# Kernel optimization log

Hardware: AMD Instinct MI355X
Metric: run time of the kernel (lower is better)

## Reference

```python
import jax, jax.numpy as jnp
import numpy as np
from jax import lax

P_BOX, N_PTS, K_MAX, HID, SAMP = 512, 50000, 64, 256, 4
C_IMG, HF, WF = 96, 160, 512
IMG_W, IMG_H = 1280.0, 384.0
OFFSET_SCALE = 0.04
PT_IN = 7


def _lin(key, fan_in, fan_out):
    return jax.random.normal(key, (fan_in, fan_out), dtype=jnp.float32) / np.sqrt(fan_in)


def setup_inputs() -> dict:
    key = jax.random.key(0)
    ks = jax.random.split(key, 24)
    xy = jax.random.uniform(ks[0], (N_PTS, 2), minval=-40.0, maxval=40.0)
    z = jax.random.uniform(ks[1], (N_PTS, 1), minval=-2.0, maxval=4.0)
    feats = jax.random.normal(ks[2], (N_PTS, 4))
    points = jnp.concatenate([xy, z, feats], axis=-1).astype(jnp.float32)
    ctr_xy = jax.random.uniform(ks[3], (P_BOX, 2), minval=-35.0, maxval=35.0)
    ctr_z = jax.random.uniform(ks[4], (P_BOX, 1), minval=-1.0, maxval=2.0)
    dxy = jax.random.uniform(ks[5], (P_BOX, 2), minval=2.0, maxval=6.0)
    dz = jax.random.uniform(ks[6], (P_BOX, 1), minval=1.0, maxval=3.0)
    yaw = jax.random.uniform(ks[7], (P_BOX, 1), minval=-np.pi, maxval=np.pi)
    boxes = jnp.concatenate([ctr_xy, ctr_z, dxy, dz, yaw], axis=-1).astype(jnp.float32)
    image_feat = jax.random.normal(ks[8], (1, C_IMG, HF, WF), dtype=jnp.float32)
    fx = fy = 400.0
    proj = jnp.array([[IMG_W / 2, -fx, 0.0, 0.0], [IMG_H / 2, 0.0, -fy, 0.0], [1.0, 0.0, 0.0, 0.0]], dtype=jnp.float32)
    return {
        'points': points, 'boxes': boxes, 'image_feat': image_feat, 'proj': proj,
        'pe_w1': _lin(ks[9], PT_IN + 1, HID), 'pe_b1': jnp.zeros((HID,), jnp.float32),
        'pe_w2': _lin(ks[10], HID, HID), 'pe_b2': jnp.zeros((HID,), jnp.float32),
        'q_w': _lin(ks[11], HID, HID), 'q_b': jnp.zeros((HID,), jnp.float32),
        'f_w': _lin(ks[12], C_IMG, HID), 'f_b': jnp.zeros((HID,), jnp.float32),
        'off_w': _lin(ks[13], HID, SAMP * 2), 'off_b': jnp.zeros((SAMP * 2,), jnp.float32),
        'wt_w': _lin(ks[14], HID, SAMP), 'wt_b': jnp.zeros((SAMP,), jnp.float32),
        'o_w1': _lin(ks[15], 2 * HID, HID), 'o_b1': jnp.zeros((HID,), jnp.float32),
        'o_w2': _lin(ks[16], HID, HID), 'o_b2': jnp.zeros((HID,), jnp.float32),
        'score_w': _lin(ks[17], HID, 1), 'score_b': jnp.zeros((1,), jnp.float32),
    }


def _fused_features(points, boxes, image_feat, proj, pe_w1, pe_b1, pe_w2, pe_b2,
                    q_w, q_b, f_w, f_b, off_w, off_b, wt_w, wt_b,
                    o_w1, o_b1, o_w2, o_b2, score_w, score_b):
    NEG = jnp.float32(-1e30)
    xyz = points[:, :3]
    ctr, dims, yaw = boxes[:, :3], boxes[:, 3:6], boxes[:, 6]
    c, s = jnp.cos(yaw)[:, None], jnp.sin(yaw)[:, None]
    rel = xyz[None, :, :] - ctr[:, None, :]                      # [P,N,3]
    lx = rel[..., 0] * c + rel[..., 1] * s                       # box-frame coords
    ly = -rel[..., 0] * s + rel[..., 1] * c
    lz = rel[..., 2]
    half = dims[:, None, :] * 0.5
    inside = (jnp.abs(lx) <= half[..., 0]) & (jnp.abs(ly) <= half[..., 1]) & (jnp.abs(lz) <= half[..., 2])
    counts = inside.sum(axis=1)                                  # [P]
    d = jnp.maximum(dims, 1e-3)[:, None, :]
    nx, ny, nz = lx / d[..., 0], ly / d[..., 1], lz / d[..., 2] - 0.5
    planar = jnp.where(inside, jnp.sqrt(nx * nx + ny * ny), jnp.inf)
    _, idx = lax.top_k(-planar, K_MAX)                           # K closest inside points
    slot_valid = jnp.arange(K_MAX)[None, :] < counts[:, None]    # [P,K]
    take = lambda a: jnp.take_along_axis(a, idx, axis=1)
    nl = jnp.stack([take(nx), take(ny), take(nz)], axis=-1)      # [P,K,3]
    nl = jnp.where(slot_valid[..., None], nl, 0.0)
    pts_sel = jnp.where(slot_valid[..., None], points[idx], 0.0)  # [P,K,7]
    # local density: knn(4) mean distance, excluding self
    diff = nl[:, :, None, :] - nl[:, None, :, :]
    dmat = jnp.sqrt((diff * diff).sum(-1) + 1e-12)               # [P,K,K]
    dmat = jnp.where(slot_valid[:, None, :], dmat, jnp.inf)
    knn = -lax.top_k(-dmat, 4)[0]                                # 4 smallest, col0 = self
    m = jnp.minimum(counts, K_MAX)
    col_ok = jnp.arange(1, 4)[None, None, :] < jnp.minimum(m, 4)[:, None, None]
    nb = jnp.where(col_ok, knn[:, :, 1:], 0.0)
    n_nb = jnp.maximum(jnp.minimum(m, 4) - 1, 1).astype(nl.dtype)
    density = jnp.where(slot_valid, jnp.exp(-nb.sum(-1) / n_nb[:, None]), 0.0)  # [P,K]
    tokens = jnp.concatenate([nl, pts_sel[:, :, 3:PT_IN], density[..., None]], axis=-1)  # [P,K,8]
    h = jnp.maximum(tokens @ pe_w1 + pe_b1, 0.0) @ pe_w2 + pe_b2  # point encoder [P,K,H]
    # project points to normalized image coords
    hom = pts_sel[:, :, :3] @ proj[:, :3].T + proj[:, 3]
    depth = hom[..., 2]
    safe_d = jnp.where(jnp.abs(depth) > 1e-3, depth, 1e-3)
    rx = 2.0 * (hom[..., 0] / safe_d) / (IMG_W - 1.0) - 1.0
    ry = 2.0 * (hom[..., 1] / safe_d) / (IMG_H - 1.0) - 1.0
    ref = jnp.stack([rx, ry], axis=-1)                           # [P,K,2]
    valid = (depth > 0.1) & (jnp.abs(rx) <= 1.0) & (jnp.abs(ry) <= 1.0) & slot_valid
    # cross-modal deformable attention (lite)
    q = h @ q_w + q_b
    fm = jnp.einsum('chw,cd->dhw', image_feat[0], f_w) + f_b[:, None, None]  # [H,Hf,Wf]
    offs = (jnp.tanh(h @ off_w + off_b)).reshape(P_BOX, K_MAX, SAMP, 2) * OFFSET_SCALE
    w = jax.nn.softmax(h @ wt_w + wt_b, axis=-1)                 # [P,K,S]
    grid = jnp.clip(ref[:, :, None, :] + offs, -1.2, 1.2)
    px = (grid[..., 0] + 1.0) * 0.5 * (WF - 1)                   # align_corners=True
    py = (grid[..., 1] + 1.0) * 0.5 * (HF - 1)
    x0, y0 = jnp.floor(px), jnp.floor(py)

    def gather(xi, yi):
        inb = (xi >= 0) & (xi <= WF - 1) & (yi >= 0) & (yi <= HF - 1)
        xc = jnp.clip(xi, 0, WF - 1).astype(jnp.int32)
        yc = jnp.clip(yi, 0, HF - 1).astype(jnp.int32)
        return fm[:, yc, xc] * inb[None].astype(fm.dtype)        # [H,P,K,S]

    wx1, wy1 = px - x0, py - y0
    samp = (gather(x0, y0) * (1 - wx1) * (1 - wy1) + gather(x0 + 1, y0) * wx1 * (1 - wy1)
            + gather(x0, y0 + 1) * (1 - wx1) * wy1 + gather(x0 + 1, y0 + 1) * wx1 * wy1)
    samp = jnp.moveaxis(samp, 0, -1)                             # [P,K,S,H]
    vm = valid.astype(h.dtype)
    samp = samp * vm[:, :, None, None]
    w = w * vm[:, :, None]
    w = w / jnp.maximum(w.sum(-1, keepdims=True), 1e-6)
    context = (samp * w[..., None]).sum(axis=2) * vm[..., None]  # [P,K,H]
    cat = jnp.concatenate([q * vm[..., None], context], axis=-1)
    img_tok = jnp.maximum(cat @ o_w1 + o_b1, 0.0) @ o_w2 + o_b2
    fused = h + img_tok                                          # [P,K,H]
    # masked attention pooling over valid slots
    logits = (fused @ score_w + score_b).squeeze(-1)
    logits = jnp.where(slot_valid, logits, NEG)
    valid_rows = slot_valid.any(axis=1)
    logits = jnp.where(valid_rows[:, None], logits, 0.0)
    pw = jnp.where(valid_rows[:, None], jax.nn.softmax(logits, axis=-1), 0.0)
    pooled = jnp.einsum('pk,pkd->pd', pw, fused)                 # [P,H]
    return pooled, counts.astype(jnp.float32)[:, None]


def reference(points, boxes, image_feat, proj, pe_w1, pe_b1, pe_w2, pe_b2,
              q_w, q_b, f_w, f_b, off_w, off_b, wt_w, wt_b,
              o_w1, o_b1, o_w2, o_b2, score_w, score_b):
    return _fused_features(points, boxes, image_feat, proj, pe_w1, pe_b1, pe_w2, pe_b2,
                           q_w, q_b, f_w, f_b, off_w, off_b, wt_w, wt_b,
                           o_w1, o_b1, o_w2, o_b2, score_w, score_b)
```

## Files before the change

### kernel.cpp

```cpp
#include <hip/hip_runtime.h>
#include <hip/hip_bf16.h>

#define P_BOX 512
#define NP    50000
#define NPAD  50176
#define KM    64
#define NKEY  4096
#define HF    160
#define WF    512

typedef unsigned long long u64;
typedef unsigned short u16;
typedef unsigned int u32;
typedef __attribute__((ext_vector_type(8))) short short8;
typedef __attribute__((ext_vector_type(4))) float f32x4;

__device__ __forceinline__ u16 f2bf(float f) {
  u32 u = __float_as_uint(f);
  u32 r = u + 0x7fffu + ((u >> 16) & 1u);
  return (u16)(r >> 16);
}
__device__ __forceinline__ float bf2f(u16 h) { return __uint_as_float(((u32)h) << 16); }
__device__ __forceinline__ float bfl(u32 u) { return __uint_as_float(u << 16); }
__device__ __forceinline__ float bfh(u32 u) { return __uint_as_float(u & 0xffff0000u); }

__device__ __forceinline__ int aIdx(int m, int d) {
  return m * 256 + (((d >> 3) ^ (m & 7)) << 3) + (d & 7);
}
__device__ __forceinline__ const short8* aGr(const u16* A, int m, int g) {
  return (const short8*)(A + m * 256 + ((g ^ (m & 7)) << 3));
}

__launch_bounds__(512)
__global__ void k_prep(const float* __restrict__ pts, const float* __restrict__ img,
                       const float* __restrict__ q_w, const float* __restrict__ q_b,
                       const float* __restrict__ f_w, const float* __restrict__ f_b,
                       const float* __restrict__ o_w1, const float* __restrict__ pe_w1,
                       const float* __restrict__ pe_w2, const float* __restrict__ o_w2,
                       const float* __restrict__ off_w, const float* __restrict__ wt_w,
                       const float* __restrict__ off_b, const float* __restrict__ wt_b,
                       float* __restrict__ xs, float* __restrict__ ys, float* __restrict__ zs,
                       u16* __restrict__ pe_w2T, u16* __restrict__ WqT,
                       u16* __restrict__ o_w2T, u16* __restrict__ FoT,
                       u16* __restrict__ HWT, u16* __restrict__ pe_w1T,
                       float* __restrict__ bq, float* __restrict__ fbo,
                       float* __restrict__ hb, u16* __restrict__ imgT) {
  __shared__ __align__(16) char smem[99840];
  const int blk = blockIdx.x;
  const int t = threadIdx.x;

  if (blk < 160) {
    const int h = blk;
    u16* tile = (u16*)smem;
#pragma unroll 4
    for (int it = 0; it < 24; ++it) {
      int idx = it * 512 + t;
      int c = idx >> 7, w4 = idx & 127;
      float4 v = ((const float4*)(img + ((size_t)(c * HF + h)) * WF))[w4];
      ushort4 o;
      o.x = f2bf(v.x); o.y = f2bf(v.y); o.z = f2bf(v.z); o.w = f2bf(v.w);
      *(ushort4*)(tile + c * 520 + w4 * 4) = o;
    }
    __syncthreads();
#pragma unroll 2
    for (int it = 0; it < 12; ++it) {
      int idx = it * 512 + t;
      int w = idx / 12, cq = idx % 12;
      const u16* tp = tile + (cq * 8) * 520 + w;
      u32 p0 = (u32)tp[0] | ((u32)tp[520] << 16);
      u32 p1 = (u32)tp[1040] | ((u32)tp[1560] << 16);
      u32 p2 = (u32)tp[2080] | ((u32)tp[2600] << 16);
      u32 p3 = (u32)tp[3120] | ((u32)tp[3640] << 16);
      ((uint4*)(imgT + ((size_t)(h * WF + w)) * 96))[cq] = make_uint4(p0, p1, p2, p3);
    }
  } else if (blk < 185) {
    int g = blk - 160;
#pragma unroll
    for (int r = 0; r < 4; ++r) {
      int i = g * 2048 + r * 512 + t;
      if (i < NPAD) {
        if (i < NP) {
          xs[i] = pts[i * 7 + 0];
          ys[i] = pts[i * 7 + 1];
          zs[i] = pts[i * 7 + 2];
        } else {
          xs[i] = 1e9f; ys[i] = 1e9f; zs[i] = 1e9f;
        }
      }
    }
  } else if (blk < 209) {
    int gg = blk - 185;
    const bool isWq = gg < 16;
    const int g = isWq ? gg : gg - 16;
    const int n0 = (g & 3) * 64;
    const int x0 = (g >> 2) * 64;
    float* sA = (float*)smem;
    float* sB = (float*)smem + 64 * 65;
    float acc[2][4];
#pragma unroll
    for (int r = 0; r < 2; ++r)
#pragma unroll
      for (int c = 0; c < 4; ++c) acc[r][c] = 0.f;
    const int tx = t & 15, ty = t >> 4;
    for (int j0 = 0; j0 < 256; j0 += 64) {
      {
        int nn = t & 63, jb = t >> 6;
#pragma unroll
        for (int r = 0; r < 8; ++r) {
          int jj = jb + r * 8;
          int row = (isWq ? 0 : 256) + j0 + jj;
          sA[jj * 65 + nn] = o_w1[row * 256 + n0 + nn];
        }
      }
      {
        int jj = t & 63, xb = t >> 6;
#pragma unroll
        for (int r = 0; r < 8; ++r) {
          int xx = xb + r * 8;
          float v = 0.f;
          if (isWq) v = q_w[(x0 + xx) * 256 + j0 + jj];
          else if (x0 + xx < 96) v = f_w[(x0 + xx) * 256 + j0 + jj];
          sB[jj * 65 + xx] = v;
        }
      }
      __syncthreads();
#pragma unroll 8
      for (int jj = 0; jj < 64; ++jj) {
        float a[2], b[4];
#pragma unroll
        for (int r = 0; r < 2; ++r) a[r] = sA[jj * 65 + ty * 2 + r];
#pragma unroll
        for (int c = 0; c < 4; ++c) b[c] = sB[jj * 65 + tx * 4 + c];
#pragma unroll
        for (int r = 0; r < 2; ++r)
#pragma unroll
          for (int c = 0; c < 4; ++c) acc[r][c] += a[r] * b[c];
      }
      __syncthreads();
    }
    if (isWq) {
#pragma unroll
      for (int r = 0; r < 2; ++r) {
        ushort4 o;
        o.x = f2bf(acc[r][0]); o.y = f2bf(acc[r][1]);
        o.z = f2bf(acc[r][2]); o.w = f2bf(acc[r][3]);
        *(ushort4*)(WqT + (size_t)(n0 + ty * 2 + r) * 256 + x0 + tx * 4) = o;
      }
    } else if (x0 + tx * 4 < 96) {
#pragma unroll
      for (int r = 0; r < 2; ++r) {
        ushort4 o;
        o.x = f2bf(acc[r][0]); o.y = f2bf(acc[r][1]);
        o.z = f2bf(acc[r][2]); o.w = f2bf(acc[r][3]);
        *(ushort4*)(FoT + (size_t)(n0 + ty * 2 + r) * 96 + x0 + tx * 4) = o;
      }
    }
  } else if (blk < 241) {
    int g = blk - 209;
    const float* src = (g < 16) ? pe_w2 : o_w2;
    u16* dst = (g < 16) ? pe_w2T : o_w2T;
    int tile_ = g & 15;
    int n0 = (tile_ & 3) * 64, k0 = (tile_ >> 2) * 64;
    float* shf = (float*)smem;
    {
      int nn = t & 63, kb = t >> 6;
#pragma unroll
      for (int r = 0; r < 8; ++r) {
        int kk = kb + r * 8;
        shf[kk * 65 + nn] = src[(k0 + kk) * 256 + n0 + nn];
      }
    }
    __syncthreads();
    {
      int kk = t & 63, nb = t >> 6;
#pragma unroll
      for (int r = 0; r < 8; ++r) {
        int nn = nb + r * 8;
        dst[(size_t)(n0 + nn) * 256 + k0 + kk] = f2bf(shf[kk * 65 + nn]);
      }
    }
  } else {
    if (t < 256) {
      int n = t;
      float a1 = 0.f, a2 = 0.f;
      for (int j = 0; j < 256; ++j) {
        a1 += q_b[j] * o_w1[j * 256 + n];
        a2 += f_b[j] * o_w1[(256 + j) * 256 + n];
      }
      bq[n] = a1;
      fbo[n] = a2;
#pragma unroll
      for (int s = 0; s < 16; ++s) {
        float v = (s < 8) ? off_w[n * 8 + s] : ((s < 12) ? wt_w[n * 4 + (s - 8)] : 0.f);
        HWT[s * 256 + n] = f2bf(v);
      }
#pragma unroll
      for (int k = 0; k < 32; ++k)
        pe_w1T[n * 32 + k] = (k < 8) ? f2bf(pe_w1[k * 256 + n]) : (u16)0;
      if (t < 16) hb[t] = (t < 8) ? off_b[t] : ((t < 12) ? wt_b[t - 8] : 0.f);
    }
  }
}

__launch_bounds__(512)
__global__ void k_sel(const float* __restrict__ pts, const float* __restrict__ boxes,
                      const float* __restrict__ proj,
                      const float* __restrict__ xs, const float* __restrict__ ys,
                      const float* __restrict__ zs,
                      uint4* __restrict__ TOK, float* __restrict__ VM,
                      float* __restrict__ REF, int* __restrict__ CNT,
                      float* __restrict__ out) {
  __shared__ u64 keys[NKEY];
  __shared__ u64 keys2[KM];
  __shared__ float s_nl[KM * 3], s_ft[KM * 4];
  __shared__ float s_knn[KM * 32];
  __shared__ int cntp;

  const int p = blockIdx.x;
  const int tid = threadIdx.x;

  const float cx = boxes[p * 7 + 0], cy = boxes[p * 7 + 1], cz = boxes[p * 7 + 2];
  const float dx = boxes[p * 7 + 3], dy = boxes[p * 7 + 4], dz = boxes[p * 7 + 5];
  const float yaw = boxes[p * 7 + 6];
  const float cth = cosf(yaw), sth = sinf(yaw);
  const float hx = dx * 0.5f, hy = dy * 0.5f, hz = dz * 0.5f;
  const float ddx = fmaxf(dx, 1e-3f), ddy = fmaxf(dy, 1e-3f), ddz = fmaxf(dz, 1e-3f);

  if (tid == 0) cntp = 0;
  __syncthreads();

  for (int i = tid * 4; i < NPAD; i += 2048) {
    float4 x4 = *(const float4*)(xs + i);
    float4 y4 = *(const float4*)(ys + i);
    float4 z4 = *(const float4*)(zs + i);
#pragma unroll
    for (int c = 0; c < 4; ++c) {
      float xv = (c == 0) ? x4.x : (c == 1) ? x4.y : (c == 2) ? x4.z : x4.w;
      float yv = (c == 0) ? y4.x : (c == 1) ? y4.y : (c == 2) ? y4.z : y4.w;
      float zv = (c == 0) ? z4.x : (c == 1) ? z4.y : (c == 2) ? z4.z : z4.w;
      float rx0 = xv - cx, ry0 = yv - cy, rz0 = zv - cz;
      float lx = rx0 * cth + ry0 * sth;
      float ly = ry0 * cth - rx0 * sth;
      if (fabsf(lx) <= hx && fabsf(ly) <= hy && fabsf(rz0) <= hz) {
        int pos = atomicAdd(&cntp, 1);
        if (pos < NKEY) {
          float nx = lx / ddx, ny = ly / ddy;
          float pl = sqrtf(nx * nx + ny * ny);
          keys[pos] = (((u64)__float_as_uint(pl)) << 32) | (u32)(i + c);
        }
      }
    }
  }
  __syncthreads();
  const int cnt = cntp;
  const int m = min(cnt, KM);

  if (cnt <= KM) {
    if (tid < cnt) keys2[tid] = keys[tid];
  } else {
    int cc = min(cnt, NKEY);
    if (cc <= 1024) {
      u64 k0v = ~0ull, k1v = ~0ull;
      bool h0 = tid < cc, h1 = tid + 512 < cc;
      if (h0) k0v = keys[tid];
      if (h1) k1v = keys[tid + 512];
      int r0 = 0, r1 = 0;
      for (int i = 0; i < cc; ++i) {
        u64 ki = keys[i];
        r0 += (ki < k0v) ? 1 : 0;
        r1 += (ki < k1v) ? 1 : 0;
      }
      if (h0 && r0 < KM) keys2[r0] = k0v;
      if (h1 && r1 < KM) keys2[r1] = k1v;
    } else {
      int nn = 2048;
      while (nn < cc) nn <<= 1;
      for (int i = cc + tid; i < nn; i += 512) keys[i] = ~0ull;
      __syncthreads();
      for (int k = 2; k <= nn; k <<= 1) {
        for (int j = k >> 1; j > 0; j >>= 1) {
          for (int t = tid; t < nn; t += 512) {
            int ixj = t ^ j;
            if (ixj > t) {
              u64 a = keys[t], b = keys[ixj];
              bool up = ((t & k) == 0);
              if ((a > b) == up) { keys[t] = b; keys[ixj] = a; }
            }
          }
          __syncthreads();
        }
      }
      if (tid < KM) keys2[tid] = keys[tid];
    }
  }
  __syncthreads();

  if (tid < KM) {
    int k = tid;
    float x = 0.f, y = 0.f, z = 0.f, n0 = 0.f, n1 = 0.f, n2 = 0.f;
    float f0 = 0.f, f1 = 0.f, f2 = 0.f, f3 = 0.f;
    if (k < m) {
      u32 pi = (u32)(keys2[k] & 0xffffffffu);
      const float* pp = pts + (size_t)pi * 7;
      x = pp[0]; y = pp[1]; z = pp[2];
      f0 = pp[3]; f1 = pp[4]; f2 = pp[5]; f3 = pp[6];
      float rx0 = x - cx, ry0 = y - cy, rz0 = z - cz;
      float lx = rx0 * cth + ry0 * sth;
      float ly = ry0 * cth - rx0 * sth;
      n0 = lx / ddx; n1 = ly / ddy; n2 = rz0 / ddz - 0.5f;
    }
    s_nl[k * 3 + 0] = n0; s_nl[k * 3 + 1] = n1; s_nl[k * 3 + 2] = n2;
    s_ft[k * 4 + 0] = f0; s_ft[k * 4 + 1] = f1; s_ft[k * 4 + 2] = f2; s_ft[k * 4 + 3] = f3;
    float h0 = proj[0] * x + proj[1] * y + proj[2] * z + proj[3];
    float h1 = proj[4] * x + proj[5] * y + proj[6] * z + proj[7];
    float dep = proj[8] * x + proj[9] * y + proj[10] * z + proj[11];
    float sd = (fabsf(dep) > 1e-3f) ? dep : 1e-3f;
    float rx = 2.f * (h0 / sd) / 1279.f - 1.f;
    float ry = 2.f * (h1 / sd) / 383.f - 1.f;
    bool v = (dep > 0.1f) && (fabsf(rx) <= 1.f) && (fabsf(ry) <= 1.f) && (k < m);
    VM[p * KM + k] = v ? 1.f : 0.f;
    REF[p * KM * 2 + k * 2 + 0] = rx;
    REF[p * KM * 2 + k * 2 + 1] = ry;
  }
  __syncthreads();

  {
    int k = tid & 63, part = tid >> 6;
    float a0 = s_nl[k * 3], a1 = s_nl[k * 3 + 1], a2 = s_nl[k * 3 + 2];
    float b0 = 1e30f, b1 = 1e30f, b2 = 1e30f, b3 = 1e30f;
#pragma unroll
    for (int jj = 0; jj < 8; ++jj) {
      int j = part * 8 + jj;
      if (j < m) {
        float d0 = a0 - s_nl[j * 3], d1 = a1 - s_nl[j * 3 + 1], d2 = a2 - s_nl[j * 3 + 2];
        float dd = sqrtf(d0 * d0 + d1 * d1 + d2 * d2 + 1e-12f);
        if (dd < b3) {
          if (dd < b0)      { b3 = b2; b2 = b1; b1 = b0; b0 = dd; }
          else if (dd < b1) { b3 = b2; b2 = b1; b1 = dd; }
          else if (dd < b2) { b3 = b2; b2 = dd; }
          else              { b3 = dd; }
        }
      }
    }
    float* o = s_knn + k * 32 + part * 4;
    o[0] = b0; o[1] = b1; o[2] = b2; o[3] = b3;
  }
  __syncthreads();

  if (tid < KM) {
    int k = tid;
    float dens = 0.f;
    if (k < m) {
      float b0 = 1e30f, b1 = 1e30f, b2 = 1e30f, b3 = 1e30f;
#pragma unroll
      for (int i = 0; i < 32; ++i) {
        float dd = s_knn[k * 32 + i];
        if (dd < b3) {
          if (dd < b0)      { b3 = b2; b2 = b1; b1 = b0; b0 = dd; }
          else if (dd < b1) { b3 = b2; b2 = b1; b1 = dd; }
          else if (dd < b2) { b3 = b2; b2 = dd; }
          else              { b3 = dd; }
        }
      }
      int mm = min(m, 4);
      float nbs = 0.f;
      if (mm > 1) nbs += b1;
      if (mm > 2) nbs += b2;
      if (mm > 3) nbs += b3;
      dens = expf(-nbs / (float)max(mm - 1, 1));
    }
    u32 w0 = (u32)f2bf(s_nl[k * 3 + 0]) | ((u32)f2bf(s_nl[k * 3 + 1]) << 16);
    u32 w1 = (u32)f2bf(s_nl[k * 3 + 2]) | ((u32)f2bf(s_ft[k * 4 + 0]) << 16);
    u32 w2 = (u32)f2bf(s_ft[k * 4 + 1]) | ((u32)f2bf(s_ft[k * 4 + 2]) << 16);
    u32 w3 = (u32)f2bf(s_ft[k * 4 + 3]) | ((u32)f2bf(dens) << 16);
    TOK[p * KM + k] = make_uint4(w0, w1, w2, w3);
  }
  if (tid == 0) {
    CNT[p] = cnt;
    out[(size_t)P_BOX * 256 + p] = (float)cnt;
  }
}

__attribute__((amdgpu_flat_work_group_size(512, 512), amdgpu_waves_per_eu(4, 4)))
__global__ void k_mlp(const u16* __restrict__ pe_w1T, const float* __restrict__ pe_b1,
                      const float* __restrict__ pe_b2,
                      const float* __restrict__ o_b1, const float* __restrict__ o_b2,
                      const float* __restrict__ score_w, const float* __restrict__ score_b,
                      const u16* __restrict__ pe_w2T, const u16* __restrict__ WqT,
                      const u16* __restrict__ o_w2T, const u16* __restrict__ FoT,
                      const u16* __restrict__ HWT,
                      const float* __restrict__ bqv, const float* __restrict__ fbov,
                      const float* __restrict__ hbv,
                      const u16* __restrict__ imgT,
                      const uint4* __restrict__ TOK, const float* __restrict__ VM,
                      const float* __restrict__ REF, const int* __restrict__ CNT,
                      float* __restrict__ out) {
  __shared__ __align__(16) char smem[81920];
  u16* A1 = (u16*)smem;
  u16* A2 = (u16*)(smem + 32768);
  u16* CTX = (u16*)(smem + 65536);
  float* poolf = (float*)(smem + 65536);
  u16* s_tokb = (u16*)(poolf + 640);
  float* s_vm = (float*)(smem + 77824);
  float* s_coef = s_vm + 64;
  float* s_wl = s_coef + 64;
  float* s_ref = s_wl + 256;
  float* s_lg = s_ref + 128;
  float* s_pw = s_lg + 64;
  u16* s_offb = (u16*)(s_pw + 64);

  const int p = blockIdx.x;
  const int tid = threadIdx.x;
  const int m = min(CNT[p], KM);

  if (tid < KM) {
    int k = tid;
    uint4 tv = TOK[p * KM + k];
    uint4* tb = (uint4*)(s_tokb + k * 32);
    tb[0] = tv;
    tb[1] = make_uint4(0, 0, 0, 0);
    tb[2] = make_uint4(0, 0, 0, 0);
    tb[3] = make_uint4(0, 0, 0, 0);
    s_vm[k] = VM[p * KM + k];
    s_ref[k * 2 + 0] = REF[p * KM * 2 + k * 2 + 0];
    s_ref[k * 2 + 1] = REF[p * KM * 2 + k * 2 + 1];
  }
  __syncthreads();

  const int wv = tid >> 6, lane = tid & 63, q = lane >> 4, ln = lane & 15;
  const int n0g = wv * 32;

#pragma unroll 1
  for (int nt = 0; nt < 2; ++nt) {
    int n = n0g + nt * 16 + ln;
    f32x4 aH[4];
#pragma unroll
    for (int mt = 0; mt < 4; ++mt) aH[mt] = (f32x4)0.f;
    short8 b = *(const short8*)(pe_w1T + (size_t)n * 32 + q * 8);
#pragma unroll
    for (int mt = 0; mt < 4; ++mt) {
      short8 af = *(const short8*)(s_tokb + (ln + 16 * mt) * 32 + q * 8);
      aH[mt] = __builtin_amdgcn_mfma_f32_16x16x32_bf16(af, b, aH[mt], 0, 0, 0);
    }
    float bias = pe_b1[n];
#pragma unroll
    for (int mt = 0; mt < 4; ++mt)
#pragma unroll
      for (int r = 0; r < 4; ++r)
        A1[aIdx(mt * 16 + q * 4 + r, n)] = f2bf(fmaxf(aH[mt][r] + bias, 0.f));
  }
  __syncthreads();

#pragma unroll 1
  for (int nt = 0; nt < 2; ++nt) {
    int n = n0g + nt * 16 + ln;
    f32x4 acc[4];
#pragma unroll
    for (int mt = 0; mt < 4; ++mt) acc[mt] = (f32x4)0.f;
    const u16* B = pe_w2T + (size_t)n * 256 + q * 8;
#pragma unroll 2
    for (int ks = 0; ks < 8; ++ks) {
      short8 b = *(const short8*)(B + ks * 32);
#pragma unroll
      for (int mt = 0; mt < 4; ++mt) {
        short8 af = *aGr(A1, ln + 16 * mt, ks * 4 + q);
        acc[mt] = __builtin_amdgcn_mfma_f32_16x16x32_bf16(af, b, acc[mt], 0, 0, 0);
      }
    }
    float bias = pe_b2[n];
#pragma unroll
    for (int mt = 0; mt < 4; ++mt)
#pragma unroll
      for (int r = 0; r < 4; ++r)
        A2[aIdx(mt * 16 + q * 4 + r, n)] = f2bf(acc[mt][r] + bias);
  }
  __syncthreads();

  if (wv < 4) {
    f32x4 acc = (f32x4)0.f;
    const u16* B = HWT + (size_t)ln * 256 + q * 8;
#pragma unroll 2
    for (int ks = 0; ks < 8; ++ks) {
      short8 af = *aGr(A2, ln + 16 * wv, ks * 4 + q);
      short8 b = *(const short8*)(B + ks * 32);
      acc = __builtin_amdgcn_mfma_f32_16x16x32_bf16(af, b, acc, 0, 0, 0);
    }
    float hb_ = hbv[ln];
#pragma unroll
    for (int r = 0; r < 4; ++r) {
      int mm = wv * 16 + q * 4 + r;
      float val = acc[r] + hb_;
      if (ln < 8) s_offb[mm * 8 + ln] = f2bf(tanhf(val) * 0.04f);
      else if (ln < 12) s_wl[mm * 4 + (ln - 8)] = val;
    }
  }
  __syncthreads();

  if (tid < KM) {
    int k = tid;
    float l0 = s_wl[k * 4], l1 = s_wl[k * 4 + 1], l2 = s_wl[k * 4 + 2], l3 = s_wl[k * 4 + 3];
    float mx = fmaxf(fmaxf(l0, l1), fmaxf(l2, l3));
    float e0 = expf(l0 - mx), e1 = expf(l1 - mx), e2 = expf(l2 - mx), e3 = expf(l3 - mx);
    float si = 1.f / (e0 + e1 + e2 + e3);
    s_wl[k * 4] = e0 * si; s_wl[k * 4 + 1] = e1 * si;
    s_wl[k * 4 + 2] = e2 * si; s_wl[k * 4 + 3] = e3 * si;
  }
  __syncthreads();

  {
    int k = tid >> 3, cg = tid & 7;
    float acc[12];
#pragma unroll
    for (int c = 0; c < 12; ++c) acc[c] = 0.f;
    float coef_ = 0.f;
    if (s_vm[k] > 0.f) {
      float rx = s_ref[k * 2], ry = s_ref[k * 2 + 1];
#pragma unroll 1
      for (int s = 0; s < 4; ++s) {
        float ox = bf2f(s_offb[k * 8 + s * 2]), oy = bf2f(s_offb[k * 8 + s * 2 + 1]);
        float gx = fminf(fmaxf(rx + ox, -1.2f), 1.2f);
        float gy = fminf(fmaxf(ry + oy, -1.2f), 1.2f);
        float px = (gx + 1.f) * 0.5f * 511.f;
        float py = (gy + 1.f) * 0.5f * 159.f;
        float x0f = floorf(px), y0f = floorf(py);
        float wx1 = px - x0f, wy1 = py - y0f;
        float ws_ = s_wl[k * 4 + s];
        int x0 = (int)x0f, y0 = (int)y0f;
#pragma unroll 1
        for (int t2 = 0; t2 < 4; ++t2) {
          int xi = x0 + (t2 & 1), yi = y0 + (t2 >> 1);
          if (xi >= 0 && xi <= WF - 1 && yi >= 0 && yi <= HF - 1) {
            float tw = ((t2 & 1) ? wx1 : 1.f - wx1) * ((t2 >> 1) ? wy1 : 1.f - wy1);
            float w2 = ws_ * tw;
            coef_ += w2;
            const u16* pp = imgT + ((size_t)(yi * WF + xi)) * 96 + cg * 12;
            uint2 u0 = *(const uint2*)pp;
            uint2 u1 = *(const uint2*)(pp + 4);
            uint2 u2 = *(const uint2*)(pp + 8);
            acc[0] += w2 * bfl(u0.x); acc[1] += w2 * bfh(u0.x);
            acc[2] += w2 * bfl(u0.y); acc[3] += w2 * bfh(u0.y);
            acc[4] += w2 * bfl(u1.x); acc[5] += w2 * bfh(u1.x);
            acc[6] += w2 * bfl(u1.y); acc[7] += w2 * bfh(u1.y);
            acc[8] += w2 * bfl(u2.x); acc[9] += w2 * bfh(u2.x);
            acc[10] += w2 * bfl(u2.y); acc[11] += w2 * bfh(u2.y);
          }
        }
      }
    }
    u16* cp = CTX + k * 96 + cg * 12;
    u32 o0 = (u32)f2bf(acc[0]) | ((u32)f2bf(acc[1]) << 16);
    u32 o1 = (u32)f2bf(acc[2]) | ((u32)f2bf(acc[3]) << 16);
    u32 o2 = (u32)f2bf(acc[4]) | ((u32)f2bf(acc[5]) << 16);
    u32 o3 = (u32)f2bf(acc[6]) | ((u32)f2bf(acc[7]) << 16);
    u32 o4 = (u32)f2bf(acc[8]) | ((u32)f2bf(acc[9]) << 16);
    u32 o5 = (u32)f2bf(acc[10]) | ((u32)f2bf(acc[11]) << 16);
    *(uint2*)cp = make_uint2(o0, o1);
    *(uint2*)(cp + 4) = make_uint2(o2, o3);
    *(uint2*)(cp + 8) = make_uint2(o4, o5);
    if (cg == 0) s_coef[k] = coef_;
  }
  __syncthreads();

#pragma unroll 1
  for (int nt = 0; nt < 2; ++nt) {
    int n = n0g + nt * 16 + ln;
    f32x4 aB[4];
#pragma unroll
    for (int mt = 0; mt < 4; ++mt) aB[mt] = (f32x4)0.f;
    const u16* BF = FoT + (size_t)n * 96 + q * 8;
#pragma unroll 1
    for (int ks = 0; ks < 3; ++ks) {
      short8 b = *(const short8*)(BF + ks * 32);
#pragma unroll
      for (int mt = 0; mt < 4; ++mt) {
        short8 cf = *(const short8*)(CTX + (ln + 16 * mt) * 96 + ks * 32 + q * 8);
        aB[mt] = __builtin_amdgcn_mfma_f32_16x16x32_bf16(cf, b, aB[mt], 0, 0, 0);
      }
    }
    const u16* BW = WqT + (size_t)n * 256 + q * 8;
#pragma unroll 2
    for (int ks = 0; ks < 8; ++ks) {
      short8 b = *(const short8*)(BW + ks * 32);
#pragma unroll
      for (int mt = 0; mt < 4; ++mt) {
        short8 af = *aGr(A2, ln + 16 * mt, ks * 4 + q);
        aB[mt] = __builtin_amdgcn_mfma_f32_16x16x32_bf16(af, b, aB[mt], 0, 0, 0);
      }
    }
    float fb = fbov[n], ob = o_b1[n], bq_ = bqv[n];
#pragma unroll
    for (int mt = 0; mt < 4; ++mt)
#pragma unroll
      for (int r = 0; r < 4; ++r) {
        int mm = mt * 16 + q * 4 + r;
        float val = (s_vm[mm] > 0.f) ? (aB[mt][r] + bq_ + s_coef[mm] * fb + ob) : ob;
        A1[aIdx(mm, n)] = f2bf(fmaxf(val, 0.f));
      }
  }
  __syncthreads();

#pragma unroll 1
  for (int nt = 0; nt < 2; ++nt) {
    int n = n0g + nt * 16 + ln;
    f32x4 acc[4];
#pragma unroll
    for (int mt = 0; mt < 4; ++mt) acc[mt] = (f32x4)0.f;
    const u16* B = o_w2T + (size_t)n * 256 + q * 8;
#pragma unroll 2
    for (int ks = 0; ks < 8; ++ks) {
      short8 b = *(const short8*)(B + ks * 32);
#pragma unroll
      for (int mt = 0; mt < 4; ++mt) {
        short8 af = *aGr(A1, ln + 16 * mt, ks * 4 + q);
        acc[mt] = __builtin_amdgcn_mfma_f32_16x16x32_bf16(af, b, acc[mt], 0, 0, 0);
      }
    }
    float b2 = o_b2[n];
#pragma unroll
    for (int mt = 0; mt < 4; ++mt)
#pragma unroll
      for (int r = 0; r < 4; ++r) {
        int mm = mt * 16 + q * 4 + r;
        int i0 = aIdx(mm, n);
        A2[i0] = f2bf(bf2f(A2[i0]) + acc[mt][r] + b2);
      }
  }
  __syncthreads();

  {
    int k = tid >> 3, part = tid & 7;
    float a = 0.f;
#pragma unroll 1
    for (int gi = 0; gi < 4; ++gi) {
      int g = part * 4 + gi;
      uint4 uu = *(const uint4*)aGr(A2, k, g);
      const float4* sw = (const float4*)(score_w + g * 8);
      float4 s0 = sw[0], s1 = sw[1];
      a += bfl(uu.x) * s0.x + bfh(uu.x) * s0.y + bfl(uu.y) * s0.z + bfh(uu.y) * s0.w;
      a += bfl(uu.z) * s1.x + bfh(uu.z) * s1.y + bfl(uu.w) * s1.z + bfh(uu.w) * s1.w;
    }
    poolf[k * 8 + part] = a;
  }
  __syncthreads();
  if (tid < KM) {
    float a = score_b[0];
#pragma unroll
    for (int j = 0; j < 8; ++j) a += poolf[tid * 8 + j];
    s_lg[tid] = a;
  }
  __syncthreads();

  if (wv == 0) {
    int k = lane;
    float lg = (k < m) ? s_lg[k] : -1e30f;
    float mx = lg;
#pragma unroll
    for (int o = 32; o; o >>= 1) mx = fmaxf(mx, __shfl_xor(mx, o));
    float e = (k < m) ? expf(lg - mx) : 0.f;
    float ss = e;
#pragma unroll
    for (int o = 32; o; o >>= 1) ss += __shfl_xor(ss, o);
    s_pw[k] = (m > 0 && k < m) ? e / ss : 0.f;
  }
  __syncthreads();

  if (tid < 256) {
    int d = tid;
    float acc = 0.f;
    for (int k = 0; k < KM; ++k) acc += s_pw[k] * bf2f(A2[aIdx(k, d)]);
    out[(size_t)p * 256 + d] = acc;
  }
}

extern "C" void kernel_launch(void* const* d_in, const int* in_sizes, int n_in,
                              void* d_out, int out_size, void* d_ws, size_t ws_size,
                              hipStream_t stream) {
  (void)in_sizes; (void)n_in; (void)out_size; (void)ws_size;
  const float* points  = (const float*)d_in[0];
  const float* boxes   = (const float*)d_in[1];
  const float* img     = (const float*)d_in[2];
  const float* proj    = (const float*)d_in[3];
  const float* pe_w1   = (const float*)d_in[4];
  const float* pe_b1   = (const float*)d_in[5];
  const float* pe_w2   = (const float*)d_in[6];
  const float* pe_b2   = (const float*)d_in[7];
  const float* q_w     = (const float*)d_in[8];
  const float* q_b     = (const float*)d_in[9];
  const float* f_w     = (const float*)d_in[10];
  const float* f_b     = (const float*)d_in[11];
  const float* off_w   = (const float*)d_in[12];
  const float* off_b   = (const float*)d_in[13];
  const float* wt_w    = (const float*)d_in[14];
  const float* wt_b    = (const float*)d_in[15];
  const float* o_w1    = (const float*)d_in[16];
  const float* o_b1    = (const float*)d_in[17];
  const float* o_w2    = (const float*)d_in[18];
  const float* o_b2    = (const float*)d_in[19];
  const float* score_w = (const float*)d_in[20];
  const float* score_b = (const float*)d_in[21];
  float* out = (float*)d_out;

  char* W = (char*)d_ws;
  float* xs    = (float*)(W + 0);
  float* ysv   = (float*)(W + 200704);
  float* zsv   = (float*)(W + 401408);
  float* bqv   = (float*)(W + 602112);
  float* fbov  = (float*)(W + 603136);
  float* hbv   = (float*)(W + 604160);
  u16* pe_w2T  = (u16*)(W + 604416);
  u16* WqT     = (u16*)(W + 735488);
  u16* o_w2T   = (u16*)(W + 866560);
  u16* FoT     = (u16*)(W + 997632);
  u16* HWT     = (u16*)(W + 1046784);
  u16* pe_w1T  = (u16*)(W + 1054976);
  u16* imgT    = (u16*)(W + 1071360);
  uint4* TOK   = (uint4*)(W + 16800000);
  float* VM    = (float*)(W + 17324288);
  float* REF   = (float*)(W + 17455360);
  int*   CNTW  = (int*)(W + 17717504);

  k_prep<<<243, 512, 0, stream>>>(points, img, q_w, q_b, f_w, f_b, o_w1, pe_w1, pe_w2,
                                  o_w2, off_w, wt_w, off_b, wt_b, xs, ysv, zsv,
                                  pe_w2T, WqT, o_w2T, FoT, HWT, pe_w1T, bqv, fbov, hbv, imgT);
  k_sel<<<P_BOX, 512, 0, stream>>>(points, boxes, proj, xs, ysv, zsv,
                                   TOK, VM, REF, CNTW, out);
  k_mlp<<<P_BOX, 512, 0, stream>>>(pe_w1T, pe_b1, pe_b2, o_b1, o_b2, score_w, score_b,
                                   pe_w2T, WqT, o_w2T, FoT, HWT, bqv, fbov, hbv, imgT,
                                   TOK, VM, REF, CNTW, out);
}
```

Baseline: 216.9 us.

## Split each box's MLP across two blocks and merge the pooling with a split softmax

The MLP kernel now launches two blocks per box, each handling 32 of the 64 slots with half the shared memory. Each block writes a partial softmax max, sum and weighted feature vector. A new small kernel merges the two halves with log-sum-exp rescaling. The goal is more blocks and higher occupancy on the GPU, at the cost of every block reloading the full weight matrices, writing a partial buffer, and an extra kernel launch.

Measured after the change: 236.7 us. +9.1%, slower.

```diff
diff --git a/kernel.cpp b/kernel.cpp
--- a/kernel.cpp
+++ b/kernel.cpp
@@ -381,7 +381,7 @@
   }
 }
 
-__attribute__((amdgpu_flat_work_group_size(512, 512), amdgpu_waves_per_eu(4, 4)))
+__launch_bounds__(512)
 __global__ void k_mlp(const u16* __restrict__ pe_w1T, const float* __restrict__ pe_b1,
                       const float* __restrict__ pe_b2,
                       const float* __restrict__ o_b1, const float* __restrict__ o_b2,
@@ -394,36 +394,37 @@
                       const u16* __restrict__ imgT,
                       const uint4* __restrict__ TOK, const float* __restrict__ VM,
                       const float* __restrict__ REF, const int* __restrict__ CNT,
-                      float* __restrict__ out) {
-  __shared__ __align__(16) char smem[81920];
+                      float* __restrict__ PS) {
+  __shared__ __align__(16) char smem[40704];
   u16* A1 = (u16*)smem;
-  u16* A2 = (u16*)(smem + 32768);
-  u16* CTX = (u16*)(smem + 65536);
-  float* poolf = (float*)(smem + 65536);
-  u16* s_tokb = (u16*)(poolf + 640);
-  float* s_vm = (float*)(smem + 77824);
-  float* s_coef = s_vm + 64;
-  float* s_wl = s_coef + 64;
-  float* s_ref = s_wl + 256;
-  float* s_lg = s_ref + 128;
-  float* s_pw = s_lg + 64;
-  u16* s_offb = (u16*)(s_pw + 64);
-
-  const int p = blockIdx.x;
+  u16* A2 = (u16*)(smem + 16384);
+  u16* CTX = (u16*)(smem + 32768);
+  float* poolf = (float*)(smem + 32768);
+  u16* s_tokb = (u16*)(smem + 32768);
+  float* s_vm = (float*)(smem + 38912);
+  float* s_coef = s_vm + 32;
+  float* s_wl = s_coef + 32;
+  float* s_ref = s_wl + 128;
+  float* s_lg = s_ref + 64;
+  float* s_pw = s_lg + 32;
+  u16* s_offb = (u16*)(s_pw + 32);
+
+  const int p = blockIdx.x >> 1;
+  const int R0 = (blockIdx.x & 1) * 32;
   const int tid = threadIdx.x;
   const int m = min(CNT[p], KM);
 
-  if (tid < KM) {
-    int k = tid;
-    uint4 tv = TOK[p * KM + k];
-    uint4* tb = (uint4*)(s_tokb + k * 32);
+  if (tid < 32) {
+    int kg = R0 + tid;
+    uint4 tv = TOK[p * KM + kg];
+    uint4* tb = (uint4*)(s_tokb + tid * 32);
     tb[0] = tv;
     tb[1] = make_uint4(0, 0, 0, 0);
     tb[2] = make_uint4(0, 0, 0, 0);
     tb[3] = make_uint4(0, 0, 0, 0);
-    s_vm[k] = VM[p * KM + k];
-    s_ref[k * 2 + 0] = REF[p * KM * 2 + k * 2 + 0];
-    s_ref[k * 2 + 1] = REF[p * KM * 2 + k * 2 + 1];
+    s_vm[tid] = VM[p * KM + kg];
+    s_ref[tid * 2 + 0] = REF[p * KM * 2 + kg * 2 + 0];
+    s_ref[tid * 2 + 1] = REF[p * KM * 2 + kg * 2 + 1];
   }
   __syncthreads();
 
@@ -433,18 +434,18 @@
 #pragma unroll 1
   for (int nt = 0; nt < 2; ++nt) {
     int n = n0g + nt * 16 + ln;
-    f32x4 aH[4];
-#pragma unroll
-    for (int mt = 0; mt < 4; ++mt) aH[mt] = (f32x4)0.f;
+    f32x4 aH[2];
+#pragma unroll
+    for (int mt = 0; mt < 2; ++mt) aH[mt] = (f32x4)0.f;
     short8 b = *(const short8*)(pe_w1T + (size_t)n * 32 + q * 8);
 #pragma unroll
-    for (int mt = 0; mt < 4; ++mt) {
+    for (int mt = 0; mt < 2; ++mt) {
       short8 af = *(const short8*)(s_tokb + (ln + 16 * mt) * 32 + q * 8);
       aH[mt] = __builtin_amdgcn_mfma_f32_16x16x32_bf16(af, b, aH[mt], 0, 0, 0);
     }
     float bias = pe_b1[n];
 #pragma unroll
-    for (int mt = 0; mt < 4; ++mt)
+    for (int mt = 0; mt < 2; ++mt)
 #pragma unroll
       for (int r = 0; r < 4; ++r)
         A1[aIdx(mt * 16 + q * 4 + r, n)] = f2bf(fmaxf(aH[mt][r] + bias, 0.f));
@@ -454,29 +455,29 @@
 #pragma unroll 1
   for (int nt = 0; nt < 2; ++nt) {
     int n = n0g + nt * 16 + ln;
-    f32x4 acc[4];
-#pragma unroll
-    for (int mt = 0; mt < 4; ++mt) acc[mt] = (f32x4)0.f;
+    f32x4 acc[2];
+#pragma unroll
+    for (int mt = 0; mt < 2; ++mt) acc[mt] = (f32x4)0.f;
     const u16* B = pe_w2T + (size_t)n * 256 + q * 8;
 #pragma unroll 2
     for (int ks = 0; ks < 8; ++ks) {
       short8 b = *(const short8*)(B + ks * 32);
 #pragma unroll
-      for (int mt = 0; mt < 4; ++mt) {
+      for (int mt = 0; mt < 2; ++mt) {
         short8 af = *aGr(A1, ln + 16 * mt, ks * 4 + q);
         acc[mt] = __builtin_amdgcn_mfma_f32_16x16x32_bf16(af, b, acc[mt], 0, 0, 0);
       }
     }
     float bias = pe_b2[n];
 #pragma unroll
-    for (int mt = 0; mt < 4; ++mt)
+    for (int mt = 0; mt < 2; ++mt)
 #pragma unroll
       for (int r = 0; r < 4; ++r)
         A2[aIdx(mt * 16 + q * 4 + r, n)] = f2bf(acc[mt][r] + bias);
   }
   __syncthreads();
 
-  if (wv < 4) {
+  if (wv < 2) {
     f32x4 acc = (f32x4)0.f;
     const u16* B = HWT + (size_t)ln * 256 + q * 8;
 #pragma unroll 2
@@ -496,7 +497,7 @@
   }
   __syncthreads();
 
-  if (tid < KM) {
+  if (tid < 32) {
     int k = tid;
     float l0 = s_wl[k * 4], l1 = s_wl[k * 4 + 1], l2 = s_wl[k * 4 + 2], l3 = s_wl[k * 4 + 3];
     float mx = fmaxf(fmaxf(l0, l1), fmaxf(l2, l3));
@@ -508,10 +509,10 @@
   __syncthreads();
 
   {
-    int k = tid >> 3, cg = tid & 7;
-    float acc[12];
-#pragma unroll
-    for (int c = 0; c < 12; ++c) acc[c] = 0.f;
+    int k = tid >> 4, cg = tid & 15;
+    float acc[6];
+#pragma unroll
+    for (int c = 0; c < 6; ++c) acc[c] = 0.f;
     float coef_ = 0.f;
     if (s_vm[k] > 0.f) {
       float rx = s_ref[k * 2], ry = s_ref[k * 2 + 1];
@@ -533,30 +534,19 @@
             float tw = ((t2 & 1) ? wx1 : 1.f - wx1) * ((t2 >> 1) ? wy1 : 1.f - wy1);
             float w2 = ws_ * tw;
             coef_ += w2;
-            const u16* pp = imgT + ((size_t)(yi * WF + xi)) * 96 + cg * 12;
-            uint2 u0 = *(const uint2*)pp;
-            uint2 u1 = *(const uint2*)(pp + 4);
-            uint2 u2 = *(const uint2*)(pp + 8);
-            acc[0] += w2 * bfl(u0.x); acc[1] += w2 * bfh(u0.x);
-            acc[2] += w2 * bfl(u0.y); acc[3] += w2 * bfh(u0.y);
-            acc[4] += w2 * bfl(u1.x); acc[5] += w2 * bfh(u1.x);
-            acc[6] += w2 * bfl(u1.y); acc[7] += w2 * bfh(u1.y);
-            acc[8] += w2 * bfl(u2.x); acc[9] += w2 * bfh(u2.x);
-            acc[10] += w2 * bfl(u2.y); acc[11] += w2 * bfh(u2.y);
+            const u32* pp = (const u32*)(imgT + ((size_t)(yi * WF + xi)) * 96 + cg * 6);
+            u32 u0 = pp[0], u1 = pp[1], u2 = pp[2];
+            acc[0] += w2 * bfl(u0); acc[1] += w2 * bfh(u0);
+            acc[2] += w2 * bfl(u1); acc[3] += w2 * bfh(u1);
+            acc[4] += w2 * bfl(u2); acc[5] += w2 * bfh(u2);
           }
         }
       }
     }
-    u16* cp = CTX + k * 96 + cg * 12;
-    u32 o0 = (u32)f2bf(acc[0]) | ((u32)f2bf(acc[1]) << 16);
-    u32 o1 = (u32)f2bf(acc[2]) | ((u32)f2bf(acc[3]) << 16);
-    u32 o2 = (u32)f2bf(acc[4]) | ((u32)f2bf(acc[5]) << 16);
-    u32 o3 = (u32)f2bf(acc[6]) | ((u32)f2bf(acc[7]) << 16);
-    u32 o4 = (u32)f2bf(acc[8]) | ((u32)f2bf(acc[9]) << 16);
-    u32 o5 = (u32)f2bf(acc[10]) | ((u32)f2bf(acc[11]) << 16);
-    *(uint2*)cp = make_uint2(o0, o1);
-    *(uint2*)(cp + 4) = make_uint2(o2, o3);
-    *(uint2*)(cp + 8) = make_uint2(o4, o5);
+    u32* cp = (u32*)(CTX + k * 96 + cg * 6);
+    cp[0] = (u32)f2bf(acc[0]) | ((u32)f2bf(acc[1]) << 16);
+    cp[1] = (u32)f2bf(acc[2]) | ((u32)f2bf(acc[3]) << 16);
+    cp[2] = (u32)f2bf(acc[4]) | ((u32)f2bf(acc[5]) << 16);
     if (cg == 0) s_coef[k] = coef_;
   }
   __syncthreads();
@@ -564,15 +554,15 @@
 #pragma unroll 1
   for (int nt = 0; nt < 2; ++nt) {
     int n = n0g + nt * 16 + ln;
-    f32x4 aB[4];
-#pragma unroll
-    for (int mt = 0; mt < 4; ++mt) aB[mt] = (f32x4)0.f;
+    f32x4 aB[2];
+#pragma unroll
+    for (int mt = 0; mt < 2; ++mt) aB[mt] = (f32x4)0.f;
     const u16* BF = FoT + (size_t)n * 96 + q * 8;
 #pragma unroll 1
     for (int ks = 0; ks < 3; ++ks) {
       short8 b = *(const short8*)(BF + ks * 32);
 #pragma unroll
-      for (int mt = 0; mt < 4; ++mt) {
+      for (int mt = 0; mt < 2; ++mt) {
         short8 cf = *(const short8*)(CTX + (ln + 16 * mt) * 96 + ks * 32 + q * 8);
         aB[mt] = __builtin_amdgcn_mfma_f32_16x16x32_bf16(cf, b, aB[mt], 0, 0, 0);
       }
@@ -582,14 +572,14 @@
     for (int ks = 0; ks < 8; ++ks) {
       short8 b = *(const short8*)(BW + ks * 32);
 #pragma unroll
-      for (int mt = 0; mt < 4; ++mt) {
+      for (int mt = 0; mt < 2; ++mt) {
         short8 af = *aGr(A2, ln + 16 * mt, ks * 4 + q);
         aB[mt] = __builtin_amdgcn_mfma_f32_16x16x32_bf16(af, b, aB[mt], 0, 0, 0);
       }
     }
     float fb = fbov[n], ob = o_b1[n], bq_ = bqv[n];
 #pragma unroll
-    for (int mt = 0; mt < 4; ++mt)
+    for (int mt = 0; mt < 2; ++mt)
 #pragma unroll
       for (int r = 0; r < 4; ++r) {
         int mm = mt * 16 + q * 4 + r;
@@ -602,22 +592,22 @@
 #pragma unroll 1
   for (int nt = 0; nt < 2; ++nt) {
     int n = n0g + nt * 16 + ln;
-    f32x4 acc[4];
-#pragma unroll
-    for (int mt = 0; mt < 4; ++mt) acc[mt] = (f32x4)0.f;
+    f32x4 acc[2];
+#pragma unroll
+    for (int mt = 0; mt < 2; ++mt) acc[mt] = (f32x4)0.f;
     const u16* B = o_w2T + (size_t)n * 256 + q * 8;
 #pragma unroll 2
     for (int ks = 0; ks < 8; ++ks) {
       short8 b = *(const short8*)(B + ks * 32);
 #pragma unroll
-      for (int mt = 0; mt < 4; ++mt) {
+      for (int mt = 0; mt < 2; ++mt) {
         short8 af = *aGr(A1, ln + 16 * mt, ks * 4 + q);
         acc[mt] = __builtin_amdgcn_mfma_f32_16x16x32_bf16(af, b, acc[mt], 0, 0, 0);
       }
     }
     float b2 = o_b2[n];
 #pragma unroll
-    for (int mt = 0; mt < 4; ++mt)
+    for (int mt = 0; mt < 2; ++mt)
 #pragma unroll
       for (int r = 0; r < 4; ++r) {
         int mm = mt * 16 + q * 4 + r;
@@ -627,7 +617,7 @@
   }
   __syncthreads();
 
-  {
+  if (tid < 256) {
     int k = tid >> 3, part = tid & 7;
     float a = 0.f;
 #pragma unroll 1
@@ -642,34 +632,49 @@
     poolf[k * 8 + part] = a;
   }
   __syncthreads();
-  if (tid < KM) {
+  if (tid < 32) {
     float a = score_b[0];
 #pragma unroll
     for (int j = 0; j < 8; ++j) a += poolf[tid * 8 + j];
-    s_lg[tid] = a;
-  }
-  __syncthreads();
-
-  if (wv == 0) {
-    int k = lane;
-    float lg = (k < m) ? s_lg[k] : -1e30f;
-    float mx = lg;
-#pragma unroll
-    for (int o = 32; o; o >>= 1) mx = fmaxf(mx, __shfl_xor(mx, o));
-    float e = (k < m) ? expf(lg - mx) : 0.f;
-    float ss = e;
-#pragma unroll
-    for (int o = 32; o; o >>= 1) ss += __shfl_xor(ss, o);
-    s_pw[k] = (m > 0 && k < m) ? e / ss : 0.f;
+    s_lg[tid] = (R0 + tid < m) ? a : -1e30f;
+  }
+  __syncthreads();
+
+  if (tid < 32) {
+    float mx = -1e30f;
+    for (int j = 0; j < 32; ++j) mx = fmaxf(mx, s_lg[j]);
+    float e = (R0 + tid < m) ? expf(s_lg[tid] - mx) : 0.f;
+    s_pw[tid] = e;
+    if (tid == 0) {
+      float ss = 0.f;
+      for (int j = 0; j < 32; ++j)
+        ss += (R0 + j < m) ? expf(s_lg[j] - mx) : 0.f;
+      PS[(size_t)blockIdx.x * 260 + 0] = mx;
+      PS[(size_t)blockIdx.x * 260 + 1] = ss;
+    }
   }
   __syncthreads();
 
   if (tid < 256) {
     int d = tid;
     float acc = 0.f;
-    for (int k = 0; k < KM; ++k) acc += s_pw[k] * bf2f(A2[aIdx(k, d)]);
-    out[(size_t)p * 256 + d] = acc;
-  }
+    for (int k = 0; k < 32; ++k) acc += s_pw[k] * bf2f(A2[aIdx(k, d)]);
+    PS[(size_t)blockIdx.x * 260 + 2 + d] = acc;
+  }
+}
+
+__launch_bounds__(256)
+__global__ void k_pool(const float* __restrict__ PS, float* __restrict__ out) {
+  const int p = blockIdx.x;
+  const int d = threadIdx.x;
+  const float* A = PS + (size_t)(2 * p) * 260;
+  const float* B = PS + (size_t)(2 * p + 1) * 260;
+  float mA = A[0], sA = A[1], mB = B[0], sB = B[1];
+  float mm = fmaxf(mA, mB);
+  float a = expf(mA - mm), b = expf(mB - mm);
+  float denom = a * sA + b * sB;
+  float v = a * A[2 + d] + b * B[2 + d];
+  out[(size_t)p * 256 + d] = (denom > 0.f) ? v / denom : 0.f;
 }
 
 extern "C" void kernel_launch(void* const* d_in, const int* in_sizes, int n_in,
@@ -718,13 +723,15 @@
   float* VM    = (float*)(W + 17324288);
   float* REF   = (float*)(W + 17455360);
   int*   CNTW  = (int*)(W + 17717504);
+  float* PS    = (float*)(W + 17719552);
 
   k_prep<<<243, 512, 0, stream>>>(points, img, q_w, q_b, f_w, f_b, o_w1, pe_w1, pe_w2,
                                   o_w2, off_w, wt_w, off_b, wt_b, xs, ysv, zsv,
                                   pe_w2T, WqT, o_w2T, FoT, HWT, pe_w1T, bqv, fbov, hbv, imgT);
   k_sel<<<P_BOX, 512, 0, stream>>>(points, boxes, proj, xs, ysv, zsv,
                                    TOK, VM, REF, CNTW, out);
-  k_mlp<<<P_BOX, 512, 0, stream>>>(pe_w1T, pe_b1, pe_b2, o_b1, o_b2, score_w, score_b,
-                                   pe_w2T, WqT, o_w2T, FoT, HWT, bqv, fbov, hbv, imgT,
-                                   TOK, VM, REF, CNTW, out);
+  k_mlp<<<P_BOX * 2, 512, 0, stream>>>(pe_w1T, pe_b1, pe_b2, o_b1, o_b2, score_w, score_b,
+                                       pe_w2T, WqT, o_w2T, FoT, HWT, bqv, fbov, hbv, imgT,
+                                       TOK, VM, REF, CNTW, PS);
+  k_pool<<<P_BOX, 256, 0, stream>>>(PS, out);
 }
```
